# Kernel optimization log

Measured on AMD Instinct MI355X. Metric: run time of the kernel, lower is better.

Reference implementation:

```python
import jax, jax.numpy as jnp
import numpy as np

N = 100000   # nodes
DEG = 16     # in-degree per node
E = N * DEG  # edges
D = 64       # embedding_dim


def mobius_addition(x, y, c):
    xy = jnp.sum(x * y, axis=-1, keepdims=True)
    x2 = jnp.sum(x * x, axis=-1, keepdims=True)
    y2 = jnp.sum(y * y, axis=-1, keepdims=True)
    num = (1 + 2 * c * xy + c * y2) * x + (1 - c * x2) * y
    den = 1 + 2 * c * xy + c * c * x2 * y2
    return num / den


def exp_map(x, v, c):
    vn = jnp.linalg.norm(v, axis=-1, keepdims=True)
    sc = jnp.sqrt(c)
    second = jnp.tanh(sc * vn / 2) * v / (sc * vn)
    return mobius_addition(x, second, c)


def log_map(x, y, c):
    add = mobius_addition(-x, y, c)
    an = jnp.linalg.norm(add, axis=-1, keepdims=True)
    sc = jnp.sqrt(c)
    return 2 / sc * jnp.arctanh(sc * an) * add / an


def setup_inputs() -> dict:
    key = jax.random.key(0)
    ks = jax.random.split(key, 6)
    # scale so points are well inside the Poincare ball (atanh domain)
    x = jax.random.normal(ks[0], (N, D), jnp.float32) * 0.01
    src = jax.random.randint(ks[1], (E,), 0, N, dtype=jnp.int32)
    # every node gets exactly DEG in-edges -> no isolated nodes (avoids 0/0 in exp_map)
    dst = jnp.repeat(jnp.arange(N, dtype=jnp.int32), DEG)
    s = 1.0 / np.sqrt(D)
    Wq = jax.random.normal(ks[2], (D, D), jnp.float32) * s
    Wk = jax.random.normal(ks[3], (D, D), jnp.float32) * s
    Wv = jax.random.normal(ks[4], (D, D), jnp.float32) * s
    bq = jnp.zeros((D,), jnp.float32)
    bk = jnp.zeros((D,), jnp.float32)
    bv = jnp.zeros((D,), jnp.float32)
    curvature = jnp.ones((1,), jnp.float32)
    return {"x": x, "curvature": curvature, "Wq": Wq, "bq": bq, "Wk": Wk,
            "bk": bk, "Wv": Wv, "bv": bv, "src": src, "dst": dst}


def reference(x, curvature, Wq, bq, Wk, bk, Wv, bv, src, dst):
    c = curvature  # (1,), broadcasts against (N,1) keepdim norms
    n = x.shape[0]
    origin = jnp.zeros_like(x[:1])  # (1, D)
    tangent = log_map(origin, x, c)  # (N, D)
    # torch nn.Linear: y = x @ W.T + b
    q = tangent @ Wq.T + bq
    k = tangent @ Wk.T + bk
    v = tangent @ Wv.T + bv
    scale = jnp.asarray(x.shape[-1] ** 0.5, x.dtype)
    # per-edge score: <k[src], q[dst]> / sqrt(d)
    scores = jnp.einsum('ed,ed->e', k[src], q[dst]) / scale  # (E,)
    # segment (per-dst) softmax over incoming edges
    smax = jax.ops.segment_max(scores, dst, num_segments=n)
    ex = jnp.exp(scores - smax[dst])
    ssum = jax.ops.segment_sum(ex, dst, num_segments=n)
    alpha = ex / ssum[dst]  # (E,)
    # weighted scatter-sum of src values
    h = jax.ops.segment_sum(alpha[:, None] * v[src], dst, num_segments=n)  # (N, D)
    return exp_map(origin, h, c)
```

## Files before the change

### kernel.cpp

```cpp
#include <hip/hip_runtime.h>
#include <hip/hip_bf16.h>
#include <math.h>


typedef __attribute__((ext_vector_type(8))) short bf16x8;
typedef __attribute__((ext_vector_type(4))) float f32x4;
typedef __attribute__((ext_vector_type(2))) float f32x2;

static __device__ __forceinline__ short f2bf(float f) {
    union { __hip_bfloat16 h; short s; } u; u.h = __float2bfloat16(f); return u.s;
}
static __device__ __forceinline__ float bflo(unsigned u) {
    return __uint_as_float(u << 16);
}
static __device__ __forceinline__ float bfhi(unsigned u) {
    return __uint_as_float(u & 0xffff0000u);
}

#define UBCVT(F, SRC, IDX) asm("v_cvt_f32_ubyte" IDX " %0, %1" : "=v"(F) : "v"(SRC))

#define TSTRIDE 72
#define SQSTR   72
#define SKSTR   72
#define SVSTR   68

__global__ __launch_bounds__(768) void wprep_kernel(
    const float* __restrict__ Wq, const float* __restrict__ bq,
    const float* __restrict__ Wk, const float* __restrict__ bk,
    const float* __restrict__ Wv, const float* __restrict__ bv,
    unsigned short* __restrict__ wf, float* __restrict__ bfA)
{
    const int t = threadIdx.x;
    const int tile = t >> 6, lane = t & 63;
    const int n16 = lane & 15, quad = lane >> 4;
    const int mat = tile >> 2, col0 = (tile & 3) * 16;
    const float* Wm = (mat == 0) ? Wq : (mat == 1) ? Wk : Wv;
    const float* bm = (mat == 0) ? bq : (mat == 1) ? bk : bv;
    const float* srcp = Wm + (col0 + n16) * 64 + quad * 8;
    unsigned short* dst = wf + ((size_t)tile * 64 + lane) * 16;
    #pragma unroll
    for (int h = 0; h < 2; ++h) {
        float4 a = *(const float4*)(srcp + h * 32);
        float4 b = *(const float4*)(srcp + h * 32 + 4);
        bf16x8 f;
        f[0]=f2bf(a.x); f[1]=f2bf(a.y); f[2]=f2bf(a.z); f[3]=f2bf(a.w);
        f[4]=f2bf(b.x); f[5]=f2bf(b.y); f[6]=f2bf(b.z); f[7]=f2bf(b.w);
        *(bf16x8*)(dst + h * 8) = f;
    }
    if (lane < 16) bfA[tile * 16 + lane] = bm[col0 + lane];
}

__global__ __launch_bounds__(256) void qkv_kernel(
    const float* __restrict__ x,
    const float* __restrict__ cur,
    const unsigned short* __restrict__ wf, const float* __restrict__ bfA,
    unsigned short* __restrict__ qb, unsigned char* __restrict__ kvl,
    float* __restrict__ vs, int N)
{
    __shared__ short tL[64 * TSTRIDE];
    __shared__ short sq[2][16 * SQSTR];
    __shared__ unsigned char sk[2][16 * SKSTR];
    __shared__ float svf[2][16 * SVSTR];
    const int tid = threadIdx.x;
    const int w = tid >> 6, lane = tid & 63;
    const int blockBase = blockIdx.x * 64;
    const float sc = __builtin_amdgcn_sqrtf(cur[0]);

    const int rr = lane >> 2, p = lane & 3;
    {
        const int rloc = w * 16 + rr;
        int row = blockBase + rloc; if (row >= N) row = N - 1;
        const float4* xr = (const float4*)(x + (size_t)row * 64 + p * 16);
        float4 x0 = xr[0], x1 = xr[1], x2 = xr[2], x3 = xr[3];
        float pn = x0.x*x0.x + x0.y*x0.y + x0.z*x0.z + x0.w*x0.w
                 + x1.x*x1.x + x1.y*x1.y + x1.z*x1.z + x1.w*x1.w
                 + x2.x*x2.x + x2.y*x2.y + x2.z*x2.z + x2.w*x2.w
                 + x3.x*x3.x + x3.y*x3.y + x3.z*x3.z + x3.w*x3.w;
        pn += __shfl_xor(pn, 1, 64);
        pn += __shfl_xor(pn, 2, 64);
        float z = sc * __builtin_amdgcn_sqrtf(pn);
        float ts = (z > 1e-12f)
            ? (__logf((1.0f + z) * __builtin_amdgcn_rcpf(1.0f - z))
               * __builtin_amdgcn_rcpf(z))
            : 2.0f;
        bf16x8 t0, t1;
        t0[0]=f2bf(ts*x0.x); t0[1]=f2bf(ts*x0.y); t0[2]=f2bf(ts*x0.z); t0[3]=f2bf(ts*x0.w);
        t0[4]=f2bf(ts*x1.x); t0[5]=f2bf(ts*x1.y); t0[6]=f2bf(ts*x1.z); t0[7]=f2bf(ts*x1.w);
        t1[0]=f2bf(ts*x2.x); t1[1]=f2bf(ts*x2.y); t1[2]=f2bf(ts*x2.z); t1[3]=f2bf(ts*x2.w);
        t1[4]=f2bf(ts*x3.x); t1[5]=f2bf(ts*x3.y); t1[6]=f2bf(ts*x3.z); t1[7]=f2bf(ts*x3.w);
        bf16x8* dst = (bf16x8*)&tL[rloc * TSTRIDE + p * 16];
        dst[0] = t0; dst[1] = t1;
    }

    const int n16 = lane & 15, quad = lane >> 4;
    bf16x8 Bf[3][2];
    float bias[3];
    int matv[3], col0v[3];
    #pragma unroll
    for (int tt = 0; tt < 3; ++tt) {
        const int tile = w * 3 + tt;
        matv[tt] = tile >> 2;
        col0v[tt] = (tile & 3) * 16;
        const uint4* wp = (const uint4*)(wf + ((size_t)tile * 64 + lane) * 16);
        uint4 f0 = wp[0], f1 = wp[1];
        Bf[tt][0] = *(bf16x8*)&f0;
        Bf[tt][1] = *(bf16x8*)&f1;
        bias[tt] = bfA[tile * 16 + n16];
    }
    __syncthreads();

    const int crow = tid >> 4;
    const int c8   = tid & 15;

    for (int nt = 0; nt < 4; ++nt) {
        const int b = nt & 1;
        const short* ar = &tL[(nt * 16 + n16) * TSTRIDE + quad * 8];
        bf16x8 A0 = *(const bf16x8*)ar;
        bf16x8 A1 = *(const bf16x8*)(ar + 32);
        #pragma unroll
        for (int tt = 0; tt < 3; ++tt) {
            f32x4 acc = { bias[tt], bias[tt], bias[tt], bias[tt] };
            acc = __builtin_amdgcn_mfma_f32_16x16x32_bf16(A0, Bf[tt][0], acc, 0, 0, 0);
            acc = __builtin_amdgcn_mfma_f32_16x16x32_bf16(A1, Bf[tt][1], acc, 0, 0, 0);
            const int mat = matv[tt], col0 = col0v[tt];
            #pragma unroll
            for (int r4 = 0; r4 < 4; ++r4) {
                const int rl = quad * 4 + r4;
                const int c  = col0 + n16;
                if (mat == 0) {
                    sq[b][rl * SQSTR + c] = f2bf(acc[r4]);
                } else if (mat == 1) {
                    int pk = __builtin_amdgcn_cvt_pk_fp8_f32(acc[r4], acc[r4], 0, false);
                    sk[b][rl * SKSTR + c] = (unsigned char)(pk & 0xff);
                } else {
                    svf[b][rl * SVSTR + c] = acc[r4];
                }
            }
        }
        __syncthreads();

        const int node = blockBase + nt * 16 + crow;
        {
            f32x4 v4 = *(const f32x4*)&svf[b][crow * SVSTR + c8 * 4];
            float m = fmaxf(fmaxf(fabsf(v4[0]), fabsf(v4[1])),
                            fmaxf(fabsf(v4[2]), fabsf(v4[3])));
            m = fmaxf(m, __shfl_xor(m, 1, 64));
            m = fmaxf(m, __shfl_xor(m, 2, 64));
            m = fmaxf(m, __shfl_xor(m, 4, 64));
            m = fmaxf(m, __shfl_xor(m, 8, 64));
            float rm = fmaxf(m, 1e-20f);
            float inv = 127.0f * __builtin_amdgcn_rcpf(rm);
            float scale = rm * (1.0f / 127.0f);
            int i0 = __float2int_rn(v4[0] * inv) + 128;
            int i1 = __float2int_rn(v4[1] * inv) + 128;
            int i2 = __float2int_rn(v4[2] * inv) + 128;
            int i3 = __float2int_rn(v4[3] * inv) + 128;
            unsigned pk = (unsigned)(i0 & 255) | ((unsigned)(i1 & 255) << 8)
                        | ((unsigned)(i2 & 255) << 16) | ((unsigned)(i3 & 255) << 24);
            if (node < N) {
                *(uint2*)(qb + (size_t)node * 64 + c8 * 4) =
                    *(const uint2*)&sq[b][crow * SQSTR + c8 * 4];
                *(unsigned*)(kvl + (size_t)node * 128 + c8 * 4) =
                    *(const unsigned*)&sk[b][crow * SKSTR + c8 * 4];
                *(unsigned*)(kvl + (size_t)node * 128 + 64 + c8 * 4) = pk;
                if (c8 == 0) vs[node] = scale;
            }
        }
    }
}

__global__ __launch_bounds__(256) void attn_kernel(
    const unsigned short* __restrict__ qb, const unsigned char* __restrict__ kvl,
    const float* __restrict__ vs, const int* __restrict__ src,
    const float* __restrict__ cur,
    float* __restrict__ out, int N)
{
    __shared__ float aA[4][2][16];
    const int tid = threadIdx.x;
    const int w = tid >> 6, lane = tid & 63;
    const int wg = blockIdx.x * 4 + w;
    const int stride = gridDim.x * 8;

    const int j = lane >> 2, p = lane & 3;
    const int g = lane >> 4, m = lane & 15;
    const float c0 = cur[0];
    const float sc = __builtin_amdgcn_sqrtf(c0);
    const unsigned dimoff = (unsigned)(m << 2);

    int n0 = wg * 2;
    if (n0 >= N) return;

    int  sjA0 = src[n0 * 16 + j];
    int  sjA1 = src[n0 * 16 + 16 + j];
    int4 s4A0 = *(const int4*)(src + n0 * 16 + (g << 2));
    int4 s4A1 = *(const int4*)(src + n0 * 16 + 16 + (g << 2));

    while (true) {
        const int n1 = n0 + 1;
        const int nn = n0 + stride;
        const int sj0 = sjA0, sj1 = sjA1;
        const int4 s40 = s4A0, s41 = s4A1;

        const unsigned vo00 = ((unsigned)s40.x << 7) + dimoff;
        const unsigned vo01 = ((unsigned)s40.y << 7) + dimoff;
        const unsigned vo02 = ((unsigned)s40.z << 7) + dimoff;
        const unsigned vo03 = ((unsigned)s40.w << 7) + dimoff;
        const unsigned vr00 = *(const unsigned*)(kvl + 64 + vo00);
        const unsigned vr01 = *(const unsigned*)(kvl + 64 + vo01);
        const unsigned vr02 = *(const unsigned*)(kvl + 64 + vo02);
        const unsigned vr03 = *(const unsigned*)(kvl + 64 + vo03);
        const unsigned vo10 = ((unsigned)s41.x << 7) + dimoff;
        const unsigned vo11 = ((unsigned)s41.y << 7) + dimoff;
        const unsigned vo12 = ((unsigned)s41.z << 7) + dimoff;
        const unsigned vo13 = ((unsigned)s41.w << 7) + dimoff;
        const unsigned vr10 = *(const unsigned*)(kvl + 64 + vo10);
        const unsigned vr11 = *(const unsigned*)(kvl + 64 + vo11);
        const unsigned vr12 = *(const unsigned*)(kvl + 64 + vo12);
        const unsigned vr13 = *(const unsigned*)(kvl + 64 + vo13);

        const unsigned ko0 = ((unsigned)sj0 << 7) + (unsigned)(p << 4);
        const unsigned ko1 = ((unsigned)sj1 << 7) + (unsigned)(p << 4);
        const uint4 kd0 = *(const uint4*)(kvl + ko0);
        const uint4 kd1 = *(const uint4*)(kvl + ko1);
        const float sjs0 = vs[sj0];
        const float sjs1 = vs[sj1];

        const uint4* qp0 = (const uint4*)(qb + (size_t)n0 * 64 + (p << 4));
        const uint4 qa0 = qp0[0], qc0 = qp0[1];
        const uint4* qp1 = (const uint4*)(qb + (size_t)n1 * 64 + (p << 4));
        const uint4 qa1 = qp1[0], qc1 = qp1[1];

        int sjB0, sjB1; int4 s4B0, s4B1;
        const bool more = (nn < N);
        if (more) {
            sjB0 = src[nn * 16 + j];
            sjB1 = src[nn * 16 + 16 + j];
            s4B0 = *(const int4*)(src + nn * 16 + (g << 2));
            s4B1 = *(const int4*)(src + nn * 16 + 16 + (g << 2));
        }

        float acc0 = 0.f;
        {
            f32x2 k0 = __builtin_amdgcn_cvt_pk_f32_fp8(kd0.x, false);
            f32x2 k1 = __builtin_amdgcn_cvt_pk_f32_fp8(kd0.x, true);
            acc0 = fmaf(k0[0], bflo(qa0.x), acc0); acc0 = fmaf(k0[1], bfhi(qa0.x), acc0);
            acc0 = fmaf(k1[0], bflo(qa0.y), acc0); acc0 = fmaf(k1[1], bfhi(qa0.y), acc0);
            k0 = __builtin_amdgcn_cvt_pk_f32_fp8(kd0.y, false);
            k1 = __builtin_amdgcn_cvt_pk_f32_fp8(kd0.y, true);
            acc0 = fmaf(k0[0], bflo(qa0.z), acc0); acc0 = fmaf(k0[1], bfhi(qa0.z), acc0);
            acc0 = fmaf(k1[0], bflo(qa0.w), acc0); acc0 = fmaf(k1[1], bfhi(qa0.w), acc0);
            k0 = __builtin_amdgcn_cvt_pk_f32_fp8(kd0.z, false);
            k1 = __builtin_amdgcn_cvt_pk_f32_fp8(kd0.z, true);
            acc0 = fmaf(k0[0], bflo(qc0.x), acc0); acc0 = fmaf(k0[1], bfhi(qc0.x), acc0);
            acc0 = fmaf(k1[0], bflo(qc0.y), acc0); acc0 = fmaf(k1[1], bfhi(qc0.y), acc0);
            k0 = __builtin_amdgcn_cvt_pk_f32_fp8(kd0.w, false);
            k1 = __builtin_amdgcn_cvt_pk_f32_fp8(kd0.w, true);
            acc0 = fmaf(k0[0], bflo(qc0.z), acc0); acc0 = fmaf(k0[1], bfhi(qc0.z), acc0);
            acc0 = fmaf(k1[0], bflo(qc0.w), acc0); acc0 = fmaf(k1[1], bfhi(qc0.w), acc0);
        }
        acc0 += __shfl_xor(acc0, 1, 64);
        acc0 += __shfl_xor(acc0, 2, 64);
        float ex0 = __builtin_amdgcn_exp2f(acc0 * (0.125f * 1.44269504f));
        float ss0 = ex0;
        #pragma unroll
        for (int mm = 4; mm < 64; mm <<= 1) ss0 += __shfl_xor(ss0, mm, 64);
        float as0 = ex0 * sjs0 * __builtin_amdgcn_rcpf(ss0);
        if (p == 0) aA[w][0][j] = as0;

        float acc1 = 0.f;
        {
            f32x2 k0 = __builtin_amdgcn_cvt_pk_f32_fp8(kd1.x, false);
            f32x2 k1 = __builtin_amdgcn_cvt_pk_f32_fp8(kd1.x, true);
            acc1 = fmaf(k0[0], bflo(qa1.x), acc1); acc1 = fmaf(k0[1], bfhi(qa1.x), acc1);
            acc1 = fmaf(k1[0], bflo(qa1.y), acc1); acc1 = fmaf(k1[1], bfhi(qa1.y), acc1);
            k0 = __builtin_amdgcn_cvt_pk_f32_fp8(kd1.y, false);
            k1 = __builtin_amdgcn_cvt_pk_f32_fp8(kd1.y, true);
            acc1 = fmaf(k0[0], bflo(qa1.z), acc1); acc1 = fmaf(k0[1], bfhi(qa1.z), acc1);
            acc1 = fmaf(k1[0], bflo(qa1.w), acc1); acc1 = fmaf(k1[1], bfhi(qa1.w), acc1);
            k0 = __builtin_amdgcn_cvt_pk_f32_fp8(kd1.z, false);
            k1 = __builtin_amdgcn_cvt_pk_f32_fp8(kd1.z, true);
            acc1 = fmaf(k0[0], bflo(qc1.x), acc1); acc1 = fmaf(k0[1], bfhi(qc1.x), acc1);
            acc1 = fmaf(k1[0], bflo(qc1.y), acc1); acc1 = fmaf(k1[1], bfhi(qc1.y), acc1);
            k0 = __builtin_amdgcn_cvt_pk_f32_fp8(kd1.w, false);
            k1 = __builtin_amdgcn_cvt_pk_f32_fp8(kd1.w, true);
            acc1 = fmaf(k0[0], bflo(qc1.z), acc1); acc1 = fmaf(k0[1], bfhi(qc1.z), acc1);
            acc1 = fmaf(k1[0], bflo(qc1.w), acc1); acc1 = fmaf(k1[1], bfhi(qc1.w), acc1);
        }
        acc1 += __shfl_xor(acc1, 1, 64);
        acc1 += __shfl_xor(acc1, 2, 64);
        float ex1 = __builtin_amdgcn_exp2f(acc1 * (0.125f * 1.44269504f));
        float ss1 = ex1;
        #pragma unroll
        for (int mm = 4; mm < 64; mm <<= 1) ss1 += __shfl_xor(ss1, mm, 64);
        float as1 = ex1 * sjs1 * __builtin_amdgcn_rcpf(ss1);
        if (p == 0) aA[w][1][j] = as1;

        __builtin_amdgcn_wave_barrier();
        const float4 a40 = *(const float4*)&aA[w][0][g << 2];
        const float4 a41 = *(const float4*)&aA[w][1][g << 2];
        __builtin_amdgcn_wave_barrier();
        const float sa0 = (a40.x + a40.y) + (a40.z + a40.w);
        const float sa1 = (a41.x + a41.y) + (a41.z + a41.w);

        float h00 = 0.f, h01 = 0.f, h02 = 0.f, h03 = 0.f;
        float h10 = 0.f, h11 = 0.f, h12 = 0.f, h13 = 0.f;
        {
            float f0, f1, f2, f3;
            UBCVT(f0, vr00, "0"); UBCVT(f1, vr00, "1"); UBCVT(f2, vr00, "2"); UBCVT(f3, vr00, "3");
            h00 = fmaf(a40.x, f0, h00); h01 = fmaf(a40.x, f1, h01);
            h02 = fmaf(a40.x, f2, h02); h03 = fmaf(a40.x, f3, h03);
            UBCVT(f0, vr01, "0"); UBCVT(f1, vr01, "1"); UBCVT(f2, vr01, "2"); UBCVT(f3, vr01, "3");
            h00 = fmaf(a40.y, f0, h00); h01 = fmaf(a40.y, f1, h01);
            h02 = fmaf(a40.y, f2, h02); h03 = fmaf(a40.y, f3, h03);
            UBCVT(f0, vr02, "0"); UBCVT(f1, vr02, "1"); UBCVT(f2, vr02, "2"); UBCVT(f3, vr02, "3");
            h00 = fmaf(a40.z, f0, h00); h01 = fmaf(a40.z, f1, h01);
            h02 = fmaf(a40.z, f2, h02); h03 = fmaf(a40.z, f3, h03);
            UBCVT(f0, vr03, "0"); UBCVT(f1, vr03, "1"); UBCVT(f2, vr03, "2"); UBCVT(f3, vr03, "3");
            h00 = fmaf(a40.w, f0, h00); h01 = fmaf(a40.w, f1, h01);
            h02 = fmaf(a40.w, f2, h02); h03 = fmaf(a40.w, f3, h03);

            UBCVT(f0, vr10, "0"); UBCVT(f1, vr10, "1"); UBCVT(f2, vr10, "2"); UBCVT(f3, vr10, "3");
            h10 = fmaf(a41.x, f0, h10); h11 = fmaf(a41.x, f1, h11);
            h12 = fmaf(a41.x, f2, h12); h13 = fmaf(a41.x, f3, h13);
            UBCVT(f0, vr11, "0"); UBCVT(f1, vr11, "1"); UBCVT(f2, vr11, "2"); UBCVT(f3, vr11, "3");
            h10 = fmaf(a41.y, f0, h10); h11 = fmaf(a41.y, f1, h11);
            h12 = fmaf(a41.y, f2, h12); h13 = fmaf(a41.y, f3, h13);
            UBCVT(f0, vr12, "0"); UBCVT(f1, vr12, "1"); UBCVT(f2, vr12, "2"); UBCVT(f3, vr12, "3");
            h10 = fmaf(a41.z, f0, h10); h11 = fmaf(a41.z, f1, h11);
            h12 = fmaf(a41.z, f2, h12); h13 = fmaf(a41.z, f3, h13);
            UBCVT(f0, vr13, "0"); UBCVT(f1, vr13, "1"); UBCVT(f2, vr13, "2"); UBCVT(f3, vr13, "3");
            h10 = fmaf(a41.w, f0, h10); h11 = fmaf(a41.w, f1, h11);
            h12 = fmaf(a41.w, f2, h12); h13 = fmaf(a41.w, f3, h13);
        }
        const float cr0 = 128.0f * sa0;
        const float cr1 = 128.0f * sa1;
        h00 -= cr0; h01 -= cr0; h02 -= cr0; h03 -= cr0;
        h10 -= cr1; h11 -= cr1; h12 -= cr1; h13 -= cr1;

        h00 += __shfl_xor(h00, 16, 64); h01 += __shfl_xor(h01, 16, 64);
        h02 += __shfl_xor(h02, 16, 64); h03 += __shfl_xor(h03, 16, 64);
        h10 += __shfl_xor(h10, 16, 64); h11 += __shfl_xor(h11, 16, 64);
        h12 += __shfl_xor(h12, 16, 64); h13 += __shfl_xor(h13, 16, 64);
        h00 += __shfl_xor(h00, 32, 64); h01 += __shfl_xor(h01, 32, 64);
        h02 += __shfl_xor(h02, 32, 64); h03 += __shfl_xor(h03, 32, 64);
        h10 += __shfl_xor(h10, 32, 64); h11 += __shfl_xor(h11, 32, 64);
        h12 += __shfl_xor(h12, 32, 64); h13 += __shfl_xor(h13, 32, 64);

        float n20 = h00*h00 + h01*h01 + h02*h02 + h03*h03;
        float n21 = h10*h10 + h11*h11 + h12*h12 + h13*h13;
        n20 += __shfl_xor(n20, 1, 64); n21 += __shfl_xor(n21, 1, 64);
        n20 += __shfl_xor(n20, 2, 64); n21 += __shfl_xor(n21, 2, 64);
        n20 += __shfl_xor(n20, 4, 64); n21 += __shfl_xor(n21, 4, 64);
        n20 += __shfl_xor(n20, 8, 64); n21 += __shfl_xor(n21, 8, 64);
        float z0 = sc * __builtin_amdgcn_sqrtf(n20);
        float z1 = sc * __builtin_amdgcn_sqrtf(n21);
        float e0 = __builtin_amdgcn_exp2f(z0 * 1.44269504f);
        float e1 = __builtin_amdgcn_exp2f(z1 * 1.44269504f);
        float sc0 = (z0 > 1e-12f)
            ? ((e0 - 1.0f) * __builtin_amdgcn_rcpf(z0 * (e0 + 1.0f))) : 0.5f;
        float sc1 = (z1 > 1e-12f)
            ? ((e1 - 1.0f) * __builtin_amdgcn_rcpf(z1 * (e1 + 1.0f))) : 0.5f;
        if (lane < 16) {
            float4 o0 = make_float4(sc0 * h00, sc0 * h01, sc0 * h02, sc0 * h03);
            float4 o1 = make_float4(sc1 * h10, sc1 * h11, sc1 * h12, sc1 * h13);
            *(float4*)(out + (size_t)n0 * 64 + (lane << 2)) = o0;
            *(float4*)(out + (size_t)n1 * 64 + (lane << 2)) = o1;
        }

        if (!more) break;
        n0 = nn;
        sjA0 = sjB0; sjA1 = sjB1; s4A0 = s4B0; s4A1 = s4B1;
    }
}

extern "C" void kernel_launch(void* const* d_in, const int* in_sizes, int n_in,
                              void* d_out, int out_size, void* d_ws, size_t ws_size,
                              hipStream_t stream)
{
    const float* x   = (const float*)d_in[0];
    const float* cur = (const float*)d_in[1];
    const float* Wq  = (const float*)d_in[2];
    const float* bq  = (const float*)d_in[3];
    const float* Wk  = (const float*)d_in[4];
    const float* bk  = (const float*)d_in[5];
    const float* Wv  = (const float*)d_in[6];
    const float* bv  = (const float*)d_in[7];
    const int* src = (const int*)d_in[8];

    const int N = in_sizes[0] / 64;

    unsigned short* qb  = (unsigned short*)d_ws;
    unsigned char*  kvl = (unsigned char*)(qb + (size_t)N * 64);
    float*          vsc = (float*)(kvl + (size_t)N * 128);
    unsigned short* wf  = (unsigned short*)(vsc + N);
    float*          bfA = (float*)(wf + 12 * 64 * 16);

    const int blocks1 = (N + 63) / 64;
    int blocks2 = 2048;
    const int need = (N + 7) / 8;
    if (blocks2 > need) blocks2 = need;
    wprep_kernel<<<1, 768, 0, stream>>>(Wq, bq, Wk, bk, Wv, bv, wf, bfA);
    qkv_kernel<<<blocks1, 256, 0, stream>>>(x, cur, wf, bfA, qb, kvl, vsc, N);
    attn_kernel<<<blocks2, 256, 0, stream>>>(qb, kvl, vsc, src, cur,
                                             (float*)d_out, N);
}
```

Measured before the change: 150.2 us.

## Fuse weight prep, QKV projection and attention into one persistent kernel

Merges the three launches into a single persistent kernel of 1024 blocks. Each block converts the weights to bf16 itself, loops over 64-node chunks for the QKV projection, then passes a global atomic grid barrier before running the attention phase. This removes two kernel launches and the inter-kernel gaps, but adds a memset, a spin barrier, and redundant weight conversion in every block. The barrier relies on all 1024 blocks being co-resident (launch_bounds 256,4), which is not guaranteed and could deadlock.

After: 249.5 us. +66.0%, slower.

```diff
diff --git a/kernel.cpp b/kernel.cpp
--- a/kernel.cpp
+++ b/kernel.cpp
@@ -24,73 +24,27 @@
 #define SKSTR   72
 #define SVSTR   68
 
-__global__ __launch_bounds__(768) void wprep_kernel(
+__global__ __launch_bounds__(256, 4) void fused_kernel(
+    const float* __restrict__ x,
+    const float* __restrict__ cur,
     const float* __restrict__ Wq, const float* __restrict__ bq,
     const float* __restrict__ Wk, const float* __restrict__ bk,
     const float* __restrict__ Wv, const float* __restrict__ bv,
-    unsigned short* __restrict__ wf, float* __restrict__ bfA)
-{
-    const int t = threadIdx.x;
-    const int tile = t >> 6, lane = t & 63;
-    const int n16 = lane & 15, quad = lane >> 4;
-    const int mat = tile >> 2, col0 = (tile & 3) * 16;
-    const float* Wm = (mat == 0) ? Wq : (mat == 1) ? Wk : Wv;
-    const float* bm = (mat == 0) ? bq : (mat == 1) ? bk : bv;
-    const float* srcp = Wm + (col0 + n16) * 64 + quad * 8;
-    unsigned short* dst = wf + ((size_t)tile * 64 + lane) * 16;
-    #pragma unroll
-    for (int h = 0; h < 2; ++h) {
-        float4 a = *(const float4*)(srcp + h * 32);
-        float4 b = *(const float4*)(srcp + h * 32 + 4);
-        bf16x8 f;
-        f[0]=f2bf(a.x); f[1]=f2bf(a.y); f[2]=f2bf(a.z); f[3]=f2bf(a.w);
-        f[4]=f2bf(b.x); f[5]=f2bf(b.y); f[6]=f2bf(b.z); f[7]=f2bf(b.w);
-        *(bf16x8*)(dst + h * 8) = f;
-    }
-    if (lane < 16) bfA[tile * 16 + lane] = bm[col0 + lane];
-}
-
-__global__ __launch_bounds__(256) void qkv_kernel(
-    const float* __restrict__ x,
-    const float* __restrict__ cur,
-    const unsigned short* __restrict__ wf, const float* __restrict__ bfA,
+    const int* __restrict__ src,
     unsigned short* __restrict__ qb, unsigned char* __restrict__ kvl,
-    float* __restrict__ vs, int N)
+    float* __restrict__ vs, unsigned* __restrict__ bar,
+    float* __restrict__ out, int N)
 {
     __shared__ short tL[64 * TSTRIDE];
     __shared__ short sq[2][16 * SQSTR];
     __shared__ unsigned char sk[2][16 * SKSTR];
     __shared__ float svf[2][16 * SVSTR];
+    __shared__ float aA[4][2][16];
+
     const int tid = threadIdx.x;
     const int w = tid >> 6, lane = tid & 63;
-    const int blockBase = blockIdx.x * 64;
-    const float sc = __builtin_amdgcn_sqrtf(cur[0]);
-
-    const int rr = lane >> 2, p = lane & 3;
-    {
-        const int rloc = w * 16 + rr;
-        int row = blockBase + rloc; if (row >= N) row = N - 1;
-        const float4* xr = (const float4*)(x + (size_t)row * 64 + p * 16);
-        float4 x0 = xr[0], x1 = xr[1], x2 = xr[2], x3 = xr[3];
-        float pn = x0.x*x0.x + x0.y*x0.y + x0.z*x0.z + x0.w*x0.w
-                 + x1.x*x1.x + x1.y*x1.y + x1.z*x1.z + x1.w*x1.w
-                 + x2.x*x2.x + x2.y*x2.y + x2.z*x2.z + x2.w*x2.w
-                 + x3.x*x3.x + x3.y*x3.y + x3.z*x3.z + x3.w*x3.w;
-        pn += __shfl_xor(pn, 1, 64);
-        pn += __shfl_xor(pn, 2, 64);
-        float z = sc * __builtin_amdgcn_sqrtf(pn);
-        float ts = (z > 1e-12f)
-            ? (__logf((1.0f + z) * __builtin_amdgcn_rcpf(1.0f - z))
-               * __builtin_amdgcn_rcpf(z))
-            : 2.0f;
-        bf16x8 t0, t1;
-        t0[0]=f2bf(ts*x0.x); t0[1]=f2bf(ts*x0.y); t0[2]=f2bf(ts*x0.z); t0[3]=f2bf(ts*x0.w);
-        t0[4]=f2bf(ts*x1.x); t0[5]=f2bf(ts*x1.y); t0[6]=f2bf(ts*x1.z); t0[7]=f2bf(ts*x1.w);
-        t1[0]=f2bf(ts*x2.x); t1[1]=f2bf(ts*x2.y); t1[2]=f2bf(ts*x2.z); t1[3]=f2bf(ts*x2.w);
-        t1[4]=f2bf(ts*x3.x); t1[5]=f2bf(ts*x3.y); t1[6]=f2bf(ts*x3.z); t1[7]=f2bf(ts*x3.w);
-        bf16x8* dst = (bf16x8*)&tL[rloc * TSTRIDE + p * 16];
-        dst[0] = t0; dst[1] = t1;
-    }
+    const float c0 = cur[0];
+    const float sc = __builtin_amdgcn_sqrtf(c0);
 
     const int n16 = lane & 15, quad = lane >> 4;
     bf16x8 Bf[3][2];
@@ -99,92 +53,131 @@
     #pragma unroll
     for (int tt = 0; tt < 3; ++tt) {
         const int tile = w * 3 + tt;
-        matv[tt] = tile >> 2;
-        col0v[tt] = (tile & 3) * 16;
-        const uint4* wp = (const uint4*)(wf + ((size_t)tile * 64 + lane) * 16);
-        uint4 f0 = wp[0], f1 = wp[1];
-        Bf[tt][0] = *(bf16x8*)&f0;
-        Bf[tt][1] = *(bf16x8*)&f1;
-        bias[tt] = bfA[tile * 16 + n16];
+        const int mat = tile >> 2;
+        const int col0 = (tile & 3) * 16;
+        matv[tt] = mat; col0v[tt] = col0;
+        const float* Wm = (mat == 0) ? Wq : (mat == 1) ? Wk : Wv;
+        const float* bm = (mat == 0) ? bq : (mat == 1) ? bk : bv;
+        const float* srcp = Wm + (col0 + n16) * 64 + quad * 8;
+        #pragma unroll
+        for (int h = 0; h < 2; ++h) {
+            float4 a = *(const float4*)(srcp + h * 32);
+            float4 b = *(const float4*)(srcp + h * 32 + 4);
+            bf16x8 f;
+            f[0]=f2bf(a.x); f[1]=f2bf(a.y); f[2]=f2bf(a.z); f[3]=f2bf(a.w);
+            f[4]=f2bf(b.x); f[5]=f2bf(b.y); f[6]=f2bf(b.z); f[7]=f2bf(b.w);
+            Bf[tt][h] = f;
+        }
+        bias[tt] = bm[col0 + n16];
+    }
+
+    const int rr = lane >> 2, p = lane & 3;
+    const int crow = tid >> 4;
+    const int c8   = tid & 15;
+    const int nChunks = (N + 63) >> 6;
+
+    for (int cb = blockIdx.x; cb < nChunks; cb += gridDim.x) {
+        const int blockBase = cb * 64;
+
+        {
+            const int rloc = w * 16 + rr;
+            int row = blockBase + rloc; if (row >= N) row = N - 1;
+            const float4* xr = (const float4*)(x + (size_t)row * 64 + p * 16);
+            float4 x0 = xr[0], x1 = xr[1], x2 = xr[2], x3 = xr[3];
+            float pn = x0.x*x0.x + x0.y*x0.y + x0.z*x0.z + x0.w*x0.w
+                     + x1.x*x1.x + x1.y*x1.y + x1.z*x1.z + x1.w*x1.w
+                     + x2.x*x2.x + x2.y*x2.y + x2.z*x2.z + x2.w*x2.w
+                     + x3.x*x3.x + x3.y*x3.y + x3.z*x3.z + x3.w*x3.w;
+            pn += __shfl_xor(pn, 1, 64);
+            pn += __shfl_xor(pn, 2, 64);
+            float z = sc * __builtin_amdgcn_sqrtf(pn);
+            float ts = (z > 1e-12f)
+                ? (__logf((1.0f + z) * __builtin_amdgcn_rcpf(1.0f - z))
+                   * __builtin_amdgcn_rcpf(z))
+                : 2.0f;
+            bf16x8 t0, t1;
+            t0[0]=f2bf(ts*x0.x); t0[1]=f2bf(ts*x0.y); t0[2]=f2bf(ts*x0.z); t0[3]=f2bf(ts*x0.w);
+            t0[4]=f2bf(ts*x1.x); t0[5]=f2bf(ts*x1.y); t0[6]=f2bf(ts*x1.z); t0[7]=f2bf(ts*x1.w);
+            t1[0]=f2bf(ts*x2.x); t1[1]=f2bf(ts*x2.y); t1[2]=f2bf(ts*x2.z); t1[3]=f2bf(ts*x2.w);
+            t1[4]=f2bf(ts*x3.x); t1[5]=f2bf(ts*x3.y); t1[6]=f2bf(ts*x3.z); t1[7]=f2bf(ts*x3.w);
+            bf16x8* dst = (bf16x8*)&tL[rloc * TSTRIDE + p * 16];
+            dst[0] = t0; dst[1] = t1;
+        }
+        __syncthreads();
+
+        for (int nt = 0; nt < 4; ++nt) {
+            const int b = nt & 1;
+            const short* ar = &tL[(nt * 16 + n16) * TSTRIDE + quad * 8];
+            bf16x8 A0 = *(const bf16x8*)ar;
+            bf16x8 A1 = *(const bf16x8*)(ar + 32);
+            #pragma unroll
+            for (int tt = 0; tt < 3; ++tt) {
+                f32x4 acc = { bias[tt], bias[tt], bias[tt], bias[tt] };
+                acc = __builtin_amdgcn_mfma_f32_16x16x32_bf16(A0, Bf[tt][0], acc, 0, 0, 0);
+                acc = __builtin_amdgcn_mfma_f32_16x16x32_bf16(A1, Bf[tt][1], acc, 0, 0, 0);
+                const int mat = matv[tt], col0 = col0v[tt];
+                #pragma unroll
+                for (int r4 = 0; r4 < 4; ++r4) {
+                    const int rl = quad * 4 + r4;
+                    const int c  = col0 + n16;
+                    if (mat == 0) {
+                        sq[b][rl * SQSTR + c] = f2bf(acc[r4]);
+                    } else if (mat == 1) {
+                        int pk = __builtin_amdgcn_cvt_pk_fp8_f32(acc[r4], acc[r4], 0, false);
+                        sk[b][rl * SKSTR + c] = (unsigned char)(pk & 0xff);
+                    } else {
+                        svf[b][rl * SVSTR + c] = acc[r4];
+                    }
+                }
+            }
+            __syncthreads();
+
+            const int node = blockBase + nt * 16 + crow;
+            {
+                f32x4 v4 = *(const f32x4*)&svf[b][crow * SVSTR + c8 * 4];
+                float m = fmaxf(fmaxf(fabsf(v4[0]), fabsf(v4[1])),
+                                fmaxf(fabsf(v4[2]), fabsf(v4[3])));
+                m = fmaxf(m, __shfl_xor(m, 1, 64));
+                m = fmaxf(m, __shfl_xor(m, 2, 64));
+                m = fmaxf(m, __shfl_xor(m, 4, 64));
+                m = fmaxf(m, __shfl_xor(m, 8, 64));
+                float rm = fmaxf(m, 1e-20f);
+                float inv = 127.0f * __builtin_amdgcn_rcpf(rm);
+                float scale = rm * (1.0f / 127.0f);
+                int i0 = __float2int_rn(v4[0] * inv) + 128;
+                int i1 = __float2int_rn(v4[1] * inv) + 128;
+                int i2 = __float2int_rn(v4[2] * inv) + 128;
+                int i3 = __float2int_rn(v4[3] * inv) + 128;
+                unsigned pk = (unsigned)(i0 & 255) | ((unsigned)(i1 & 255) << 8)
+                            | ((unsigned)(i2 & 255) << 16) | ((unsigned)(i3 & 255) << 24);
+                if (node < N) {
+                    *(uint2*)(qb + (size_t)node * 64 + c8 * 4) =
+                        *(const uint2*)&sq[b][crow * SQSTR + c8 * 4];
+                    *(unsigned*)(kvl + (size_t)node * 128 + c8 * 4) =
+                        *(const unsigned*)&sk[b][crow * SKSTR + c8 * 4];
+                    *(unsigned*)(kvl + (size_t)node * 128 + 64 + c8 * 4) = pk;
+                    if (c8 == 0) vs[node] = scale;
+                }
+            }
+        }
+    }
+
+    __syncthreads();
+    if (tid == 0) {
+        __threadfence();
+        atomicAdd(bar, 1u);
+        while (__hip_atomic_load(bar, __ATOMIC_RELAXED,
+                                 __HIP_MEMORY_SCOPE_AGENT) < gridDim.x) {
+            __builtin_amdgcn_s_sleep(2);
+        }
+        __threadfence();
     }
     __syncthreads();
 
-    const int crow = tid >> 4;
-    const int c8   = tid & 15;
-
-    for (int nt = 0; nt < 4; ++nt) {
-        const int b = nt & 1;
-        const short* ar = &tL[(nt * 16 + n16) * TSTRIDE + quad * 8];
-        bf16x8 A0 = *(const bf16x8*)ar;
-        bf16x8 A1 = *(const bf16x8*)(ar + 32);
-        #pragma unroll
-        for (int tt = 0; tt < 3; ++tt) {
-            f32x4 acc = { bias[tt], bias[tt], bias[tt], bias[tt] };
-            acc = __builtin_amdgcn_mfma_f32_16x16x32_bf16(A0, Bf[tt][0], acc, 0, 0, 0);
-            acc = __builtin_amdgcn_mfma_f32_16x16x32_bf16(A1, Bf[tt][1], acc, 0, 0, 0);
-            const int mat = matv[tt], col0 = col0v[tt];
-            #pragma unroll
-            for (int r4 = 0; r4 < 4; ++r4) {
-                const int rl = quad * 4 + r4;
-                const int c  = col0 + n16;
-                if (mat == 0) {
-                    sq[b][rl * SQSTR + c] = f2bf(acc[r4]);
-                } else if (mat == 1) {
-                    int pk = __builtin_amdgcn_cvt_pk_fp8_f32(acc[r4], acc[r4], 0, false);
-                    sk[b][rl * SKSTR + c] = (unsigned char)(pk & 0xff);
-                } else {
-                    svf[b][rl * SVSTR + c] = acc[r4];
-                }
-            }
-        }
-        __syncthreads();
-
-        const int node = blockBase + nt * 16 + crow;
-        {
-            f32x4 v4 = *(const f32x4*)&svf[b][crow * SVSTR + c8 * 4];
-            float m = fmaxf(fmaxf(fabsf(v4[0]), fabsf(v4[1])),
-                            fmaxf(fabsf(v4[2]), fabsf(v4[3])));
-            m = fmaxf(m, __shfl_xor(m, 1, 64));
-            m = fmaxf(m, __shfl_xor(m, 2, 64));
-            m = fmaxf(m, __shfl_xor(m, 4, 64));
-            m = fmaxf(m, __shfl_xor(m, 8, 64));
-            float rm = fmaxf(m, 1e-20f);
-            float inv = 127.0f * __builtin_amdgcn_rcpf(rm);
-            float scale = rm * (1.0f / 127.0f);
-            int i0 = __float2int_rn(v4[0] * inv) + 128;
-            int i1 = __float2int_rn(v4[1] * inv) + 128;
-            int i2 = __float2int_rn(v4[2] * inv) + 128;
-            int i3 = __float2int_rn(v4[3] * inv) + 128;
-            unsigned pk = (unsigned)(i0 & 255) | ((unsigned)(i1 & 255) << 8)
-                        | ((unsigned)(i2 & 255) << 16) | ((unsigned)(i3 & 255) << 24);
-            if (node < N) {
-                *(uint2*)(qb + (size_t)node * 64 + c8 * 4) =
-                    *(const uint2*)&sq[b][crow * SQSTR + c8 * 4];
-                *(unsigned*)(kvl + (size_t)node * 128 + c8 * 4) =
-                    *(const unsigned*)&sk[b][crow * SKSTR + c8 * 4];
-                *(unsigned*)(kvl + (size_t)node * 128 + 64 + c8 * 4) = pk;
-                if (c8 == 0) vs[node] = scale;
-            }
-        }
-    }
-}
-
-__global__ __launch_bounds__(256) void attn_kernel(
-    const unsigned short* __restrict__ qb, const unsigned char* __restrict__ kvl,
-    const float* __restrict__ vs, const int* __restrict__ src,
-    const float* __restrict__ cur,
-    float* __restrict__ out, int N)
-{
-    __shared__ float aA[4][2][16];
-    const int tid = threadIdx.x;
-    const int w = tid >> 6, lane = tid & 63;
     const int wg = blockIdx.x * 4 + w;
     const int stride = gridDim.x * 8;
-
-    const int j = lane >> 2, p = lane & 3;
+    const int j = lane >> 2;
     const int g = lane >> 4, m = lane & 15;
-    const float c0 = cur[0];
-    const float sc = __builtin_amdgcn_sqrtf(c0);
     const unsigned dimoff = (unsigned)(m << 2);
 
     int n0 = wg * 2;
@@ -392,15 +385,12 @@
     unsigned short* qb  = (unsigned short*)d_ws;
     unsigned char*  kvl = (unsigned char*)(qb + (size_t)N * 64);
     float*          vsc = (float*)(kvl + (size_t)N * 128);
-    unsigned short* wf  = (unsigned short*)(vsc + N);
-    float*          bfA = (float*)(wf + 12 * 64 * 16);
-
-    const int blocks1 = (N + 63) / 64;
-    int blocks2 = 2048;
-    const int need = (N + 7) / 8;
-    if (blocks2 > need) blocks2 = need;
-    wprep_kernel<<<1, 768, 0, stream>>>(Wq, bq, Wk, bk, Wv, bv, wf, bfA);
-    qkv_kernel<<<blocks1, 256, 0, stream>>>(x, cur, wf, bfA, qb, kvl, vsc, N);
-    attn_kernel<<<blocks2, 256, 0, stream>>>(qb, kvl, vsc, src, cur,
-                                             (float*)d_out, N);
-}
+    unsigned*       bar = (unsigned*)
+        (((uintptr_t)(vsc + N) + 255) & ~(uintptr_t)255);
+
+    hipMemsetAsync(bar, 0, 256, stream);
+
+    fused_kernel<<<1024, 256, 0, stream>>>(x, cur, Wq, bq, Wk, bk, Wv, bv,
+                                           src, qb, kvl, vsc, bar,
+                                           (float*)d_out, N);
+}
```
